# Optimization experiments

Hardware: AMD Instinct MI355X
Metric: run time of the kernel (lower is better)

## Reference

```python
import jax, jax.numpy as jnp
import numpy as np

DIM = 1024
NUM_HEADS = 16
EFF = NUM_HEADS // 2          # 8 effective heads
HEAD_DIM = DIM // NUM_HEADS   # 64
LAMBDA_INIT = 0.8
EPS = 1e-5
B, N = 2, 2048


def setup_inputs() -> dict:
    key = jax.random.key(0)
    ks = jax.random.split(key, 14)
    s = 0.02
    return {
        "x": jax.random.normal(ks[0], (B, N, DIM), jnp.float32),
        "Wq": jax.random.normal(ks[1], (DIM, DIM), jnp.float32) * s,
        "bq": jnp.zeros((DIM,), jnp.float32),
        "Wk": jax.random.normal(ks[2], (DIM, DIM), jnp.float32) * s,
        "bk": jnp.zeros((DIM,), jnp.float32),
        "Wv": jax.random.normal(ks[3], (DIM, DIM), jnp.float32) * s,
        "bv": jnp.zeros((DIM,), jnp.float32),
        "Wo": jax.random.normal(ks[4], (DIM, DIM), jnp.float32) * s,
        "bo": jnp.zeros((DIM,), jnp.float32),
        "g": jnp.ones((2 * HEAD_DIM,), jnp.float32),          # RMSNorm weight
        "lq1": jax.random.normal(ks[5], (HEAD_DIM,), jnp.float32) * 0.1,
        "lk1": jax.random.normal(ks[6], (HEAD_DIM,), jnp.float32) * 0.1,
        "lq2": jax.random.normal(ks[7], (HEAD_DIM,), jnp.float32) * 0.1,
        "lk2": jax.random.normal(ks[8], (HEAD_DIM,), jnp.float32) * 0.1,
    }


def reference(x, Wq, bq, Wk, bk, Wv, bv, Wo, bo, g, lq1, lk1, lq2, lk2):
    b, n, d = x.shape
    scaling = HEAD_DIM ** -0.5

    q = x @ Wq + bq                                  # (B,N,D)
    k = x @ Wk + bk
    v = x @ Wv + bv

    # split into 2*EFF heads of HEAD_DIM for q,k; EFF heads of 2*HEAD_DIM for v
    q = q.reshape(b, n, 2 * EFF, HEAD_DIM).transpose(0, 2, 1, 3) * scaling
    k = k.reshape(b, n, 2 * EFF, HEAD_DIM).transpose(0, 2, 1, 3)
    v = v.reshape(b, n, EFF, 2 * HEAD_DIM).transpose(0, 2, 1, 3)

    scores = jnp.einsum('bhnd,bhmd->bhnm', q, k)     # (B,2*EFF,N,N)
    probs = jax.nn.softmax(scores, axis=-1)
    probs = probs.reshape(b, EFF, 2, n, n)           # pair adjacent heads

    lam1 = jnp.exp(jnp.sum(lq1 * lk1))
    lam2 = jnp.exp(jnp.sum(lq2 * lk2))
    lam = lam1 - lam2 + LAMBDA_INIT

    diff = probs[:, :, 0] - lam * probs[:, :, 1]     # (B,EFF,N,N)
    out = jnp.einsum('bhnm,bhmd->bhnd', diff, v)     # (B,EFF,N,2*HEAD_DIM)

    # headwise RMSNorm over last dim (2*HEAD_DIM), in float32
    rms = jax.lax.rsqrt(jnp.mean(out * out, axis=-1, keepdims=True) + EPS)
    out = out * rms * g
    out = out * (1.0 - LAMBDA_INIT)

    out = out.transpose(0, 2, 1, 3).reshape(b, n, d)
    return out @ Wo + bo
```

## Files before the change

### kernel.cpp

```cpp
#include <hip/hip_runtime.h>


typedef unsigned short bf16;
typedef __attribute__((ext_vector_type(8))) short bf16x8;
typedef __attribute__((ext_vector_type(4))) float f32x4;

#define B_SZ   2
#define SEQ    2048
#define DMODEL 1024
#define NH     16
#define NEFF   8

__device__ __forceinline__ bf16 f2b(float f) {
  union { float f; unsigned int u; } c; c.f = f;
  unsigned int lsb = (c.u >> 16) & 1u;
  c.u += 0x7fffu + lsb;
  return (bf16)(c.u >> 16);
}

__device__ __forceinline__ void gll16(const void* g, void* l) {
  __builtin_amdgcn_global_load_lds(
      (const __attribute__((address_space(1))) void*)g,
      (__attribute__((address_space(3))) void*)l, 16, 0, 0);
}

__device__ __forceinline__ bf16x8 frag_swz(const bf16* tile, int row, int e) {
  const int idx = (row << 6) + (((e >> 3) ^ (row & 7)) << 3) + (e & 7);
  return *(const bf16x8*)(tile + idx);
}


__global__ void cast4_kernel(const float* __restrict__ in, bf16* __restrict__ out, int n4) {
  int i = blockIdx.x * blockDim.x + threadIdx.x;
  if (i >= n4) return;
  float4 v = reinterpret_cast<const float4*>(in)[i];
  unsigned long long r = (unsigned long long)f2b(v.x)
                       | ((unsigned long long)f2b(v.y) << 16)
                       | ((unsigned long long)f2b(v.z) << 32)
                       | ((unsigned long long)f2b(v.w) << 48);
  reinterpret_cast<unsigned long long*>(out)[i] = r;
}

__global__ void transpose_cast4_kernel(const float* __restrict__ W0, const float* __restrict__ W1,
                                       const float* __restrict__ W2, const float* __restrict__ W3,
                                       bf16* __restrict__ dqkv, bf16* __restrict__ dwo) {
  __shared__ float tile[64][65];
  const int z = blockIdx.z;
  const float* in = (z == 0) ? W0 : (z == 1) ? W1 : (z == 2) ? W2 : W3;
  bf16* out = (z < 3) ? (dqkv + (size_t)z * 1024 * 1024) : dwo;
  const int tx = threadIdx.x & 63;
  const int ty = threadIdx.x >> 6;
  const int bx = blockIdx.x << 6;
  const int by = blockIdx.y << 6;
  #pragma unroll
  for (int r = ty; r < 64; r += 4)
    tile[r][tx] = in[(size_t)(by + r) * DMODEL + bx + tx];
  __syncthreads();
  #pragma unroll
  for (int r = ty; r < 64; r += 4)
    out[(size_t)(bx + r) * DMODEL + by + tx] = f2b(tile[tx][r]);
}

__global__ void lambda_kernel(const float* lq1, const float* lk1,
                              const float* lq2, const float* lk2, float* out) {
  int l = threadIdx.x;
  float p1 = lq1[l] * lk1[l];
  float p2 = lq2[l] * lk2[l];
  #pragma unroll
  for (int off = 32; off; off >>= 1) {
    p1 += __shfl_down(p1, off, 64);
    p2 += __shfl_down(p2, off, 64);
  }
  if (l == 0) out[0] = __expf(p1) - __expf(p2) + 0.8f;
}

__launch_bounds__(256, 3)
__global__ void gemm_qkv(const bf16* __restrict__ A, const bf16* __restrict__ BT,
                         const float* __restrict__ bq, const float* __restrict__ bk,
                         const float* __restrict__ bv,
                         bf16* __restrict__ Qb, bf16* __restrict__ Kb, bf16* __restrict__ Vt) {
  __shared__ __align__(16) bf16 Asl[128][64];
  __shared__ __align__(16) bf16 Bsl[128][64];
  const int tid = threadIdx.x;
  const int wid = tid >> 6;
  const int lane = tid & 63;
  const int li = lane & 15;
  const int lg = lane >> 4;
  const int wm = (wid >> 1) << 6;
  const int wn = (wid & 1) << 6;
  const int bm = blockIdx.x << 7;
  const int bn = blockIdx.y << 7;
  const int sr = lane >> 3;
  const int scs = ((lane & 7) ^ sr) << 3;
  const bf16* Ag = A + ((size_t)bm << 10);
  const bf16* Bg = BT + ((size_t)bn << 10);
  f32x4 acc[4][4] = {};

  for (int k0 = 0; k0 < DMODEL; k0 += 64) {
    #pragma unroll
    for (int pass = 0; pass < 4; ++pass) {
      const int rb = (wid << 5) + (pass << 3);
      const int r = rb + sr;
      gll16(Ag + ((size_t)r << 10) + k0 + scs, &Asl[rb][0]);
      gll16(Bg + ((size_t)r << 10) + k0 + scs, &Bsl[rb][0]);
    }
    __syncthreads();
    #pragma unroll
    for (int kk = 0; kk < 2; ++kk) {
      bf16x8 af[4], bfx[4];
      #pragma unroll
      for (int mi = 0; mi < 4; ++mi)
        af[mi] = frag_swz(&Asl[0][0], wm + (mi << 4) + li, (kk << 5) + (lg << 3));
      #pragma unroll
      for (int ni = 0; ni < 4; ++ni)
        bfx[ni] = frag_swz(&Bsl[0][0], wn + (ni << 4) + li, (kk << 5) + (lg << 3));
      #pragma unroll
      for (int mi = 0; mi < 4; ++mi)
        #pragma unroll
        for (int ni = 0; ni < 4; ++ni)
          acc[mi][ni] = __builtin_amdgcn_mfma_f32_16x16x32_bf16(af[mi], bfx[ni], acc[mi][ni], 0, 0, 0);
    }
    __syncthreads();
  }

  const int seg = bn >> 10;
  #pragma unroll
  for (int ni = 0; ni < 4; ++ni) {
    const int gcol = bn + wn + (ni << 4) + li;
    const int c = gcol & 1023;
    const float bb = (seg == 0 ? bq : seg == 1 ? bk : bv)[c];
    #pragma unroll
    for (int mi = 0; mi < 4; ++mi) {
      const int rbase = bm + wm + (mi << 4) + (lg << 2);
      #pragma unroll
      for (int r = 0; r < 4; ++r) {
        const int grow = rbase + r;
        const int b = grow >> 11, n = grow & 2047;
        float v = acc[mi][ni][r] + bb;
        if (seg == 0) {
          v *= 0.18033688f;
          const int h = c >> 6, d = c & 63;
          Qb[((((size_t)(b * NH + h) << 11) + n) << 6) + d] = f2b(v);
        } else if (seg == 1) {
          const int h = c >> 6, d = c & 63;
          Kb[((((size_t)(b * NH + h) << 11) + n) << 6) + d] = f2b(v);
        } else {
          const int j = c >> 7, d = c & 127;
          Vt[((((size_t)(b * NEFF + j) << 7) + d) << 11) + n] = f2b(v);
        }
      }
    }
  }
}

__launch_bounds__(256, 2)
__global__ void gemm_out(const bf16* __restrict__ A, const bf16* __restrict__ BT,
                         const float* __restrict__ bias, float* __restrict__ out) {
  __shared__ __align__(16) bf16 Asl[64][64];
  __shared__ __align__(16) bf16 Bsl[128][64];
  const int tid = threadIdx.x;
  const int wid = tid >> 6;
  const int lane = tid & 63;
  const int li = lane & 15;
  const int lg = lane >> 4;
  const int wm = (wid >> 1) << 5;
  const int wn = (wid & 1) << 6;
  const int bm = blockIdx.x << 6;
  const int bn = blockIdx.y << 7;
  const int sr = lane >> 3;
  const int scs = ((lane & 7) ^ sr) << 3;
  const bf16* Ag = A + ((size_t)bm << 10);
  const bf16* Bg = BT + ((size_t)bn << 10);
  f32x4 acc[2][4] = {};

  for (int k0 = 0; k0 < DMODEL; k0 += 64) {
    #pragma unroll
    for (int pass = 0; pass < 2; ++pass) {
      const int rb = (wid << 4) + (pass << 3);
      const int r = rb + sr;
      gll16(Ag + ((size_t)r << 10) + k0 + scs, &Asl[rb][0]);
    }
    #pragma unroll
    for (int pass = 0; pass < 4; ++pass) {
      const int rb = (wid << 5) + (pass << 3);
      const int r = rb + sr;
      gll16(Bg + ((size_t)r << 10) + k0 + scs, &Bsl[rb][0]);
    }
    __syncthreads();
    #pragma unroll
    for (int kk = 0; kk < 2; ++kk) {
      bf16x8 af[2], bfx[4];
      #pragma unroll
      for (int mi = 0; mi < 2; ++mi)
        af[mi] = frag_swz(&Asl[0][0], wm + (mi << 4) + li, (kk << 5) + (lg << 3));
      #pragma unroll
      for (int ni = 0; ni < 4; ++ni)
        bfx[ni] = frag_swz(&Bsl[0][0], wn + (ni << 4) + li, (kk << 5) + (lg << 3));
      #pragma unroll
      for (int mi = 0; mi < 2; ++mi)
        #pragma unroll
        for (int ni = 0; ni < 4; ++ni)
          acc[mi][ni] = __builtin_amdgcn_mfma_f32_16x16x32_bf16(af[mi], bfx[ni], acc[mi][ni], 0, 0, 0);
    }
    __syncthreads();
  }

  #pragma unroll
  for (int ni = 0; ni < 4; ++ni) {
    const int gcol = bn + wn + (ni << 4) + li;
    const float bb = bias[gcol];
    #pragma unroll
    for (int mi = 0; mi < 2; ++mi) {
      const int rbase = bm + wm + (mi << 4) + (lg << 2);
      #pragma unroll
      for (int r = 0; r < 4; ++r) {
        const int grow = rbase + r;
        out[((size_t)grow << 10) + gcol] = acc[mi][ni][r] + bb;
      }
    }
  }
}

__launch_bounds__(256, 2)
__global__ void diff_attn(const bf16* __restrict__ Qb, const bf16* __restrict__ Kb,
                          const bf16* __restrict__ Vt, const float* __restrict__ gw,
                          const float* __restrict__ lam_p, bf16* __restrict__ attn_out) {
  __shared__ __align__(16) bf16 K0s[2][64][64];
  __shared__ __align__(16) bf16 K1s[2][64][64];
  __shared__ __align__(16) bf16 Vts[2][128][64];
  __shared__ __align__(16) bf16 Ps[4][2][16][64];

  const int tid = threadIdx.x;
  const int wid = tid >> 6;
  const int lane = tid & 63;
  const int li = lane & 15;
  const int lg = lane >> 4;

  const int bid = blockIdx.x;
  const int xcd = bid & 7;
  const int i6 = bid >> 3;
  const int p = (xcd << 1) + (i6 >> 5);
  const int q0 = (i6 & 31) << 6;
  const int b = p >> 3, j = p & 7;
  const int h0 = 2 * j, h1 = 2 * j + 1;

  const int sr = lane >> 3;
  const int scs = (((lane & 7) ^ sr)) << 3;

  const int qrow = q0 + (wid << 4) + li;
  const bf16* Q0g = Qb + ((((size_t)(b * NH + h0) << 11) + qrow) << 6);
  const bf16* Q1g = Qb + ((((size_t)(b * NH + h1) << 11) + qrow) << 6);
  bf16x8 aq0[2], aq1[2];
  aq0[0] = *(const bf16x8*)(Q0g + (lg << 3));
  aq0[1] = *(const bf16x8*)(Q0g + 32 + (lg << 3));
  aq1[0] = *(const bf16x8*)(Q1g + (lg << 3));
  aq1[1] = *(const bf16x8*)(Q1g + 32 + (lg << 3));

  const bf16* K0g = Kb + ((size_t)(b * NH + h0) << 17);
  const bf16* K1g = Kb + ((size_t)(b * NH + h1) << 17);
  const bf16* Vg  = Vt + ((size_t)p << 18);

  f32x4 o0[8] = {}, o1[8] = {};
  f32x4 ol0 = {}, ol1 = {};
  const bf16x8 vones = {0x3F80, 0x3F80, 0x3F80, 0x3F80, 0x3F80, 0x3F80, 0x3F80, 0x3F80};

  auto stage = [&](int bi, int t) {
    const int kv0 = t << 6;
    #pragma unroll
    for (int pass = 0; pass < 2; ++pass) {
      const int rl = (pass << 5) + (wid << 3) + sr;
      gll16(K0g + ((size_t)(kv0 + rl) << 6) + scs, &K0s[bi][(pass << 5) + (wid << 3)][0]);
      gll16(K1g + ((size_t)(kv0 + rl) << 6) + scs, &K1s[bi][(pass << 5) + (wid << 3)][0]);
    }
    #pragma unroll
    for (int pass = 0; pass < 4; ++pass) {
      const int d = (pass << 5) + (wid << 3) + sr;
      gll16(Vg + ((size_t)d << 11) + kv0 + scs, &Vts[bi][(pass << 5) + (wid << 3)][0]);
    }
  };

  const int NT = SEQ / 64;
  stage(0, 0);
  __syncthreads();

  for (int t = 0; t < NT; ++t) {
    const int cur = t & 1;
    if (t + 1 < NT) stage(cur ^ 1, t + 1);

    f32x4 s0[4] = {}, s1[4] = {};
    __builtin_amdgcn_s_setprio(1);
    #pragma unroll
    for (int kk = 0; kk < 2; ++kk) {
      #pragma unroll
      for (int ni = 0; ni < 4; ++ni) {
        bf16x8 bk0 = frag_swz(&K0s[cur][0][0], (ni << 4) + li, (kk << 5) + (lg << 3));
        s0[ni] = __builtin_amdgcn_mfma_f32_16x16x32_bf16(aq0[kk], bk0, s0[ni], 0, 0, 0);
        bf16x8 bk1 = frag_swz(&K1s[cur][0][0], (ni << 4) + li, (kk << 5) + (lg << 3));
        s1[ni] = __builtin_amdgcn_mfma_f32_16x16x32_bf16(aq1[kk], bk1, s1[ni], 0, 0, 0);
      }
    }
    __builtin_amdgcn_s_setprio(0);

    #pragma unroll
    for (int ni = 0; ni < 4; ++ni) {
      #pragma unroll
      for (int r = 0; r < 4; ++r) {
        const int pr = (lg << 2) + r;
        const int cs = ((ni << 4) + li) ^ ((pr & 7) << 3);
        Ps[wid][0][pr][cs] = f2b(__builtin_amdgcn_exp2f(s0[ni][r] - 12.0f));
        Ps[wid][1][pr][cs] = f2b(__builtin_amdgcn_exp2f(s1[ni][r] - 12.0f));
      }
    }
    bf16x8 pa0[2], pa1[2];
    pa0[0] = frag_swz(&Ps[wid][0][0][0], li, (lg << 3));
    pa0[1] = frag_swz(&Ps[wid][0][0][0], li, 32 + (lg << 3));
    pa1[0] = frag_swz(&Ps[wid][1][0][0], li, (lg << 3));
    pa1[1] = frag_swz(&Ps[wid][1][0][0], li, 32 + (lg << 3));
    __builtin_amdgcn_s_setprio(1);
    #pragma unroll
    for (int kk = 0; kk < 2; ++kk) {
      #pragma unroll
      for (int vc = 0; vc < 8; ++vc) {
        bf16x8 bv = frag_swz(&Vts[cur][0][0], (vc << 4) + li, (kk << 5) + (lg << 3));
        o0[vc] = __builtin_amdgcn_mfma_f32_16x16x32_bf16(pa0[kk], bv, o0[vc], 0, 0, 0);
        o1[vc] = __builtin_amdgcn_mfma_f32_16x16x32_bf16(pa1[kk], bv, o1[vc], 0, 0, 0);
      }
      ol0 = __builtin_amdgcn_mfma_f32_16x16x32_bf16(pa0[kk], vones, ol0, 0, 0, 0);
      ol1 = __builtin_amdgcn_mfma_f32_16x16x32_bf16(pa1[kk], vones, ol1, 0, 0, 0);
    }
    __builtin_amdgcn_s_setprio(0);
    __syncthreads();
  }

  const float lam = lam_p[0];
  float inv0[4], inv1[4];
  #pragma unroll
  for (int r = 0; r < 4; ++r) { inv0[r] = 1.f / ol0[r]; inv1[r] = 1.f / ol1[r]; }
  float ov[8][4];
  float ss[4] = {0.f, 0.f, 0.f, 0.f};
  #pragma unroll
  for (int vc = 0; vc < 8; ++vc)
    #pragma unroll
    for (int r = 0; r < 4; ++r) {
      const float v = o0[vc][r] * inv0[r] - lam * o1[vc][r] * inv1[r];
      ov[vc][r] = v;
      ss[r] += v * v;
    }
  #pragma unroll
  for (int r = 0; r < 4; ++r) {
    float v = ss[r];
    #pragma unroll
    for (int off = 1; off < 16; off <<= 1) v += __shfl_xor(v, off, 64);
    ss[r] = rsqrtf(v * (1.f / 128.f) + 1e-5f);
  }
  #pragma unroll
  for (int vc = 0; vc < 8; ++vc) {
    const float gv = gw[(vc << 4) + li];
    #pragma unroll
    for (int r = 0; r < 4; ++r) {
      const int row = q0 + (wid << 4) + (lg << 2) + r;
      const float v = ov[vc][r] * ss[r] * gv * 0.2f;
      attn_out[(((size_t)(b << 11) + row) << 10) + (j << 7) + (vc << 4) + li] = f2b(v);
    }
  }
}


extern "C" void kernel_launch(void* const* d_in, const int* in_sizes, int n_in,
                              void* d_out, int out_size, void* d_ws, size_t ws_size,
                              hipStream_t stream) {
  (void)in_sizes; (void)n_in; (void)out_size; (void)ws_size;
  const float* x   = (const float*)d_in[0];
  const float* Wq  = (const float*)d_in[1];
  const float* bq  = (const float*)d_in[2];
  const float* Wk  = (const float*)d_in[3];
  const float* bk  = (const float*)d_in[4];
  const float* Wv  = (const float*)d_in[5];
  const float* bv  = (const float*)d_in[6];
  const float* Wo  = (const float*)d_in[7];
  const float* bo  = (const float*)d_in[8];
  const float* g   = (const float*)d_in[9];
  const float* lq1 = (const float*)d_in[10];
  const float* lk1 = (const float*)d_in[11];
  const float* lq2 = (const float*)d_in[12];
  const float* lk2 = (const float*)d_in[13];

  char* ws = (char*)d_ws;
  const size_t MB = 1024 * 1024;
  bf16* xb    = (bf16*)(ws + 0 * MB);
  bf16* WqkvT = (bf16*)(ws + 8 * MB);
  bf16* WoT   = (bf16*)(ws + 14 * MB);
  bf16* Qb    = (bf16*)(ws + 16 * MB);
  bf16* Kb    = (bf16*)(ws + 24 * MB);
  bf16* Vt    = (bf16*)(ws + 32 * MB);
  bf16* attn  = (bf16*)(ws + 40 * MB);
  float* lam  = (float*)(ws + 48 * MB);

  cast4_kernel<<<4096, 256, 0, stream>>>(x, xb, (B_SZ * SEQ * DMODEL) / 4);
  transpose_cast4_kernel<<<dim3(16, 16, 4), 256, 0, stream>>>(Wq, Wk, Wv, Wo, WqkvT, WoT);
  lambda_kernel<<<1, 64, 0, stream>>>(lq1, lk1, lq2, lk2, lam);

  gemm_qkv<<<dim3(32, 24), 256, 0, stream>>>(xb, WqkvT, bq, bk, bv, Qb, Kb, Vt);
  diff_attn<<<512, 256, 0, stream>>>(Qb, Kb, Vt, g, lam, attn);
  gemm_out<<<dim3(64, 8), 256, 0, stream>>>(attn, WoT, bo, (float*)d_out);
}
```

Before: 147.4 us.

## Split each KV tile across two wave groups in diff attention, reduce via LDS

The attention kernel now launches 512 threads per block instead of 256. The two halves of each 64-key tile are handled by separate groups of four waves, each computing scores and PV products for 32 keys. After the loop, the partial O accumulators and row sums from the second group are added into the first group's registers through LDS, in several synchronized phases. This doubles the waves per block to raise occupancy and latency hiding, but adds a cross-wave reduction and extra barriers at the end.

```diff
diff --git a/kernel.cpp b/kernel.cpp
--- a/kernel.cpp
+++ b/kernel.cpp
@@ -221,20 +221,25 @@
   }
 }
 
-__launch_bounds__(256, 2)
+__launch_bounds__(512, 4)
 __global__ void diff_attn(const bf16* __restrict__ Qb, const bf16* __restrict__ Kb,
                           const bf16* __restrict__ Vt, const float* __restrict__ gw,
                           const float* __restrict__ lam_p, bf16* __restrict__ attn_out) {
   __shared__ __align__(16) bf16 K0s[2][64][64];
   __shared__ __align__(16) bf16 K1s[2][64][64];
   __shared__ __align__(16) bf16 Vts[2][128][64];
-  __shared__ __align__(16) bf16 Ps[4][2][16][64];
+  __shared__ __align__(16) char PsRaw[16384];
+
+  bf16* Pb = (bf16*)PsRaw;
+  float* xf = (float*)PsRaw;
 
   const int tid = threadIdx.x;
   const int wid = tid >> 6;
   const int lane = tid & 63;
   const int li = lane & 15;
   const int lg = lane >> 4;
+  const int slice = wid & 3;
+  const int kvh = wid >> 2;
 
   const int bid = blockIdx.x;
   const int xcd = bid & 7;
@@ -247,7 +252,7 @@
   const int sr = lane >> 3;
   const int scs = (((lane & 7) ^ sr)) << 3;
 
-  const int qrow = q0 + (wid << 4) + li;
+  const int qrow = q0 + (slice << 4) + li;
   const bf16* Q0g = Qb + ((((size_t)(b * NH + h0) << 11) + qrow) << 6);
   const bf16* Q1g = Qb + ((((size_t)(b * NH + h1) << 11) + qrow) << 6);
   bf16x8 aq0[2], aq1[2];
@@ -266,19 +271,17 @@
 
   auto stage = [&](int bi, int t) {
     const int kv0 = t << 6;
+    const int rl = (wid << 3) + sr;
+    gll16(K0g + ((size_t)(kv0 + rl) << 6) + scs, &K0s[bi][wid << 3][0]);
+    gll16(K1g + ((size_t)(kv0 + rl) << 6) + scs, &K1s[bi][wid << 3][0]);
     #pragma unroll
     for (int pass = 0; pass < 2; ++pass) {
-      const int rl = (pass << 5) + (wid << 3) + sr;
-      gll16(K0g + ((size_t)(kv0 + rl) << 6) + scs, &K0s[bi][(pass << 5) + (wid << 3)][0]);
-      gll16(K1g + ((size_t)(kv0 + rl) << 6) + scs, &K1s[bi][(pass << 5) + (wid << 3)][0]);
-    }
-    #pragma unroll
-    for (int pass = 0; pass < 4; ++pass) {
-      const int d = (pass << 5) + (wid << 3) + sr;
-      gll16(Vg + ((size_t)d << 11) + kv0 + scs, &Vts[bi][(pass << 5) + (wid << 3)][0]);
+      const int d = (pass << 6) + (wid << 3) + sr;
+      gll16(Vg + ((size_t)d << 11) + kv0 + scs, &Vts[bi][(pass << 6) + (wid << 3)][0]);
     }
   };
 
+  const int pbase = wid << 10;
   const int NT = SEQ / 64;
   stage(0, 0);
   __syncthreads();
@@ -287,80 +290,133 @@
     const int cur = t & 1;
     if (t + 1 < NT) stage(cur ^ 1, t + 1);
 
-    f32x4 s0[4] = {}, s1[4] = {};
+    f32x4 s0[2] = {}, s1[2] = {};
     __builtin_amdgcn_s_setprio(1);
     #pragma unroll
     for (int kk = 0; kk < 2; ++kk) {
       #pragma unroll
-      for (int ni = 0; ni < 4; ++ni) {
-        bf16x8 bk0 = frag_swz(&K0s[cur][0][0], (ni << 4) + li, (kk << 5) + (lg << 3));
+      for (int ni = 0; ni < 2; ++ni) {
+        const int rowB = (kvh << 5) + (ni << 4) + li;
+        bf16x8 bk0 = frag_swz(&K0s[cur][0][0], rowB, (kk << 5) + (lg << 3));
         s0[ni] = __builtin_amdgcn_mfma_f32_16x16x32_bf16(aq0[kk], bk0, s0[ni], 0, 0, 0);
-        bf16x8 bk1 = frag_swz(&K1s[cur][0][0], (ni << 4) + li, (kk << 5) + (lg << 3));
+        bf16x8 bk1 = frag_swz(&K1s[cur][0][0], rowB, (kk << 5) + (lg << 3));
         s1[ni] = __builtin_amdgcn_mfma_f32_16x16x32_bf16(aq1[kk], bk1, s1[ni], 0, 0, 0);
       }
     }
     __builtin_amdgcn_s_setprio(0);
 
     #pragma unroll
-    for (int ni = 0; ni < 4; ++ni) {
+    for (int ni = 0; ni < 2; ++ni) {
       #pragma unroll
       for (int r = 0; r < 4; ++r) {
         const int pr = (lg << 2) + r;
-        const int cs = ((ni << 4) + li) ^ ((pr & 7) << 3);
-        Ps[wid][0][pr][cs] = f2b(__builtin_amdgcn_exp2f(s0[ni][r] - 12.0f));
-        Ps[wid][1][pr][cs] = f2b(__builtin_amdgcn_exp2f(s1[ni][r] - 12.0f));
-      }
-    }
-    bf16x8 pa0[2], pa1[2];
-    pa0[0] = frag_swz(&Ps[wid][0][0][0], li, (lg << 3));
-    pa0[1] = frag_swz(&Ps[wid][0][0][0], li, 32 + (lg << 3));
-    pa1[0] = frag_swz(&Ps[wid][1][0][0], li, (lg << 3));
-    pa1[1] = frag_swz(&Ps[wid][1][0][0], li, 32 + (lg << 3));
+        const int col = (ni << 4) + li;
+        const int idx = (pr << 5) + ((((col >> 3) ^ (pr >> 2)) & 3) << 3) + (col & 7);
+        Pb[pbase + idx]       = f2b(__builtin_amdgcn_exp2f(s0[ni][r] - 12.0f));
+        Pb[pbase + 512 + idx] = f2b(__builtin_amdgcn_exp2f(s1[ni][r] - 12.0f));
+      }
+    }
+    const int ridx = (li << 5) + (((lg ^ (li >> 2)) & 3) << 3);
+    bf16x8 pa0 = *(const bf16x8*)(Pb + pbase + ridx);
+    bf16x8 pa1 = *(const bf16x8*)(Pb + pbase + 512 + ridx);
+
     __builtin_amdgcn_s_setprio(1);
     #pragma unroll
-    for (int kk = 0; kk < 2; ++kk) {
-      #pragma unroll
-      for (int vc = 0; vc < 8; ++vc) {
-        bf16x8 bv = frag_swz(&Vts[cur][0][0], (vc << 4) + li, (kk << 5) + (lg << 3));
-        o0[vc] = __builtin_amdgcn_mfma_f32_16x16x32_bf16(pa0[kk], bv, o0[vc], 0, 0, 0);
-        o1[vc] = __builtin_amdgcn_mfma_f32_16x16x32_bf16(pa1[kk], bv, o1[vc], 0, 0, 0);
-      }
-      ol0 = __builtin_amdgcn_mfma_f32_16x16x32_bf16(pa0[kk], vones, ol0, 0, 0, 0);
-      ol1 = __builtin_amdgcn_mfma_f32_16x16x32_bf16(pa1[kk], vones, ol1, 0, 0, 0);
-    }
+    for (int vc = 0; vc < 8; ++vc) {
+      bf16x8 bv = frag_swz(&Vts[cur][0][0], (vc << 4) + li, (kvh << 5) + (lg << 3));
+      o0[vc] = __builtin_amdgcn_mfma_f32_16x16x32_bf16(pa0, bv, o0[vc], 0, 0, 0);
+      o1[vc] = __builtin_amdgcn_mfma_f32_16x16x32_bf16(pa1, bv, o1[vc], 0, 0, 0);
+    }
+    ol0 = __builtin_amdgcn_mfma_f32_16x16x32_bf16(pa0, vones, ol0, 0, 0, 0);
+    ol1 = __builtin_amdgcn_mfma_f32_16x16x32_bf16(pa1, vones, ol1, 0, 0, 0);
     __builtin_amdgcn_s_setprio(0);
     __syncthreads();
   }
 
-  const float lam = lam_p[0];
-  float inv0[4], inv1[4];
-  #pragma unroll
-  for (int r = 0; r < 4; ++r) { inv0[r] = 1.f / ol0[r]; inv1[r] = 1.f / ol1[r]; }
-  float ov[8][4];
-  float ss[4] = {0.f, 0.f, 0.f, 0.f};
-  #pragma unroll
-  for (int vc = 0; vc < 8; ++vc)
+  #pragma unroll
+  for (int half = 0; half < 2; ++half) {
+    __syncthreads();
+    if (kvh == 1 && (slice >> 1) == half) {
+      #pragma unroll
+      for (int vc = 0; vc < 8; ++vc)
+        #pragma unroll
+        for (int r = 0; r < 4; ++r)
+          xf[((((slice & 1) << 4) + (lg << 2) + r) << 7) + (vc << 4) + li] = o0[vc][r];
+    }
+    __syncthreads();
+    if (kvh == 0 && (slice >> 1) == half) {
+      #pragma unroll
+      for (int vc = 0; vc < 8; ++vc)
+        #pragma unroll
+        for (int r = 0; r < 4; ++r)
+          o0[vc][r] += xf[((((slice & 1) << 4) + (lg << 2) + r) << 7) + (vc << 4) + li];
+    }
+  }
+  #pragma unroll
+  for (int half = 0; half < 2; ++half) {
+    __syncthreads();
+    if (kvh == 1 && (slice >> 1) == half) {
+      #pragma unroll
+      for (int vc = 0; vc < 8; ++vc)
+        #pragma unroll
+        for (int r = 0; r < 4; ++r)
+          xf[((((slice & 1) << 4) + (lg << 2) + r) << 7) + (vc << 4) + li] = o1[vc][r];
+    }
+    __syncthreads();
+    if (kvh == 0 && (slice >> 1) == half) {
+      #pragma unroll
+      for (int vc = 0; vc < 8; ++vc)
+        #pragma unroll
+        for (int r = 0; r < 4; ++r)
+          o1[vc][r] += xf[((((slice & 1) << 4) + (lg << 2) + r) << 7) + (vc << 4) + li];
+    }
+  }
+  __syncthreads();
+  if (kvh == 1 && li == 0) {
     #pragma unroll
     for (int r = 0; r < 4; ++r) {
-      const float v = o0[vc][r] * inv0[r] - lam * o1[vc][r] * inv1[r];
-      ov[vc][r] = v;
-      ss[r] += v * v;
-    }
-  #pragma unroll
-  for (int r = 0; r < 4; ++r) {
-    float v = ss[r];
-    #pragma unroll
-    for (int off = 1; off < 16; off <<= 1) v += __shfl_xor(v, off, 64);
-    ss[r] = rsqrtf(v * (1.f / 128.f) + 1e-5f);
-  }
-  #pragma unroll
-  for (int vc = 0; vc < 8; ++vc) {
-    const float gv = gw[(vc << 4) + li];
+      xf[(slice << 5) + (lg << 2) + r]      = ol0[r];
+      xf[(slice << 5) + 16 + (lg << 2) + r] = ol1[r];
+    }
+  }
+  __syncthreads();
+
+  if (kvh == 0) {
     #pragma unroll
     for (int r = 0; r < 4; ++r) {
-      const int row = q0 + (wid << 4) + (lg << 2) + r;
-      const float v = ov[vc][r] * ss[r] * gv * 0.2f;
-      attn_out[(((size_t)(b << 11) + row) << 10) + (j << 7) + (vc << 4) + li] = f2b(v);
+      ol0[r] += xf[(slice << 5) + (lg << 2) + r];
+      ol1[r] += xf[(slice << 5) + 16 + (lg << 2) + r];
+    }
+    const float lam = lam_p[0];
+    float inv0[4], inv1[4];
+    #pragma unroll
+    for (int r = 0; r < 4; ++r) { inv0[r] = 1.f / ol0[r]; inv1[r] = 1.f / ol1[r]; }
+    float ov[8][4];
+    float ss[4] = {0.f, 0.f, 0.f, 0.f};
+    #pragma unroll
+    for (int vc = 0; vc < 8; ++vc)
+      #pragma unroll
+      for (int r = 0; r < 4; ++r) {
+        const float v = o0[vc][r] * inv0[r] - lam * o1[vc][r] * inv1[r];
+        ov[vc][r] = v;
+        ss[r] += v * v;
+      }
+    #pragma unroll
+    for (int r = 0; r < 4; ++r) {
+      float v = ss[r];
+      #pragma unroll
+      for (int off = 1; off < 16; off <<= 1) v += __shfl_xor(v, off, 64);
+      ss[r] = rsqrtf(v * (1.f / 128.f) + 1e-5f);
+    }
+    #pragma unroll
+    for (int vc = 0; vc < 8; ++vc) {
+      const float gv = gw[(vc << 4) + li];
+      #pragma unroll
+      for (int r = 0; r < 4; ++r) {
+        const int row = q0 + (slice << 4) + (lg << 2) + r;
+        const float v = ov[vc][r] * ss[r] * gv * 0.2f;
+        attn_out[(((size_t)(b << 11) + row) << 10) + (j << 7) + (vc << 4) + li] = f2b(v);
+      }
     }
   }
 }
@@ -401,6 +457,6 @@
   lambda_kernel<<<1, 64, 0, stream>>>(lq1, lk1, lq2, lk2, lam);
 
   gemm_qkv<<<dim3(32, 24), 256, 0, stream>>>(xb, WqkvT, bq, bk, bv, Qb, Kb, Vt);
-  diff_attn<<<512, 256, 0, stream>>>(Qb, Kb, Vt, g, lam, attn);
+  diff_attn<<<512, 512, 0, stream>>>(Qb, Kb, Vt, g, lam, attn);
   gemm_out<<<dim3(64, 8), 256, 0, stream>>>(attn, WoT, bo, (float*)d_out);
 }
```

Result: slower. 171.4 us (+16.3%).

## Merge prep kernels into one launch and shrink output GEMM M-tile

Applied to the files above, without the earlier changes.

Three small preprocessing kernels (x cast, weight transpose-cast, lambda reduction) are merged into a single launch that dispatches on block index, removing two kernel launches and the gaps between them. Separately, the output projection GEMM tile is halved in M (64 to 32 rows), doubling the grid to 1024 blocks and raising the occupancy hint to 4, so the 256-CU device gets more blocks to spread. The smaller tile lowers data reuse per block, since each WoT tile is loaded twice as often.

```diff
diff --git a/kernel.cpp b/kernel.cpp
--- a/kernel.cpp
+++ b/kernel.cpp
@@ -29,49 +29,53 @@
   return *(const bf16x8*)(tile + idx);
 }
 
-
-__global__ void cast4_kernel(const float* __restrict__ in, bf16* __restrict__ out, int n4) {
-  int i = blockIdx.x * blockDim.x + threadIdx.x;
-  if (i >= n4) return;
-  float4 v = reinterpret_cast<const float4*>(in)[i];
-  unsigned long long r = (unsigned long long)f2b(v.x)
-                       | ((unsigned long long)f2b(v.y) << 16)
-                       | ((unsigned long long)f2b(v.z) << 32)
-                       | ((unsigned long long)f2b(v.w) << 48);
-  reinterpret_cast<unsigned long long*>(out)[i] = r;
-}
-
-__global__ void transpose_cast4_kernel(const float* __restrict__ W0, const float* __restrict__ W1,
-                                       const float* __restrict__ W2, const float* __restrict__ W3,
-                                       bf16* __restrict__ dqkv, bf16* __restrict__ dwo) {
-  __shared__ float tile[64][65];
-  const int z = blockIdx.z;
-  const float* in = (z == 0) ? W0 : (z == 1) ? W1 : (z == 2) ? W2 : W3;
-  bf16* out = (z < 3) ? (dqkv + (size_t)z * 1024 * 1024) : dwo;
-  const int tx = threadIdx.x & 63;
-  const int ty = threadIdx.x >> 6;
-  const int bx = blockIdx.x << 6;
-  const int by = blockIdx.y << 6;
-  #pragma unroll
-  for (int r = ty; r < 64; r += 4)
-    tile[r][tx] = in[(size_t)(by + r) * DMODEL + bx + tx];
-  __syncthreads();
-  #pragma unroll
-  for (int r = ty; r < 64; r += 4)
-    out[(size_t)(bx + r) * DMODEL + by + tx] = f2b(tile[tx][r]);
-}
-
-__global__ void lambda_kernel(const float* lq1, const float* lk1,
-                              const float* lq2, const float* lk2, float* out) {
-  int l = threadIdx.x;
-  float p1 = lq1[l] * lk1[l];
-  float p2 = lq2[l] * lk2[l];
-  #pragma unroll
-  for (int off = 32; off; off >>= 1) {
-    p1 += __shfl_down(p1, off, 64);
-    p2 += __shfl_down(p2, off, 64);
-  }
-  if (l == 0) out[0] = __expf(p1) - __expf(p2) + 0.8f;
+__global__ void prep_kernel(const float* __restrict__ x, bf16* __restrict__ xb,
+                            const float* __restrict__ W0, const float* __restrict__ W1,
+                            const float* __restrict__ W2, const float* __restrict__ W3,
+                            bf16* __restrict__ dqkv, bf16* __restrict__ dwo,
+                            const float* __restrict__ lq1, const float* __restrict__ lk1,
+                            const float* __restrict__ lq2, const float* __restrict__ lk2,
+                            float* __restrict__ lam) {
+  const int bid = blockIdx.x;
+  const int tid = threadIdx.x;
+  if (bid < 4096) {
+    const int i = (bid << 8) + tid;
+    float4 v = reinterpret_cast<const float4*>(x)[i];
+    unsigned long long r = (unsigned long long)f2b(v.x)
+                         | ((unsigned long long)f2b(v.y) << 16)
+                         | ((unsigned long long)f2b(v.z) << 32)
+                         | ((unsigned long long)f2b(v.w) << 48);
+    reinterpret_cast<unsigned long long*>(xb)[i] = r;
+  } else if (bid < 5120) {
+    __shared__ float tile[64][65];
+    const int t = bid - 4096;
+    const int z = t >> 8;
+    const int tz = t & 255;
+    const float* in = (z == 0) ? W0 : (z == 1) ? W1 : (z == 2) ? W2 : W3;
+    bf16* out = (z < 3) ? (dqkv + (size_t)z * 1024 * 1024) : dwo;
+    const int tx = tid & 63;
+    const int ty = tid >> 6;
+    const int bx = (tz & 15) << 6;
+    const int by = (tz >> 4) << 6;
+    #pragma unroll
+    for (int r = ty; r < 64; r += 4)
+      tile[r][tx] = in[(size_t)(by + r) * DMODEL + bx + tx];
+    __syncthreads();
+    #pragma unroll
+    for (int r = ty; r < 64; r += 4)
+      out[(size_t)(bx + r) * DMODEL + by + tx] = f2b(tile[tx][r]);
+  } else {
+    if (tid < 64) {
+      float p1 = lq1[tid] * lk1[tid];
+      float p2 = lq2[tid] * lk2[tid];
+      #pragma unroll
+      for (int off = 32; off; off >>= 1) {
+        p1 += __shfl_down(p1, off, 64);
+        p2 += __shfl_down(p2, off, 64);
+      }
+      if (tid == 0) lam[0] = __expf(p1) - __expf(p2) + 0.8f;
+    }
+  }
 }
 
 __launch_bounds__(256, 3)
@@ -153,30 +157,29 @@
   }
 }
 
-__launch_bounds__(256, 2)
+__launch_bounds__(256, 4)
 __global__ void gemm_out(const bf16* __restrict__ A, const bf16* __restrict__ BT,
                          const float* __restrict__ bias, float* __restrict__ out) {
-  __shared__ __align__(16) bf16 Asl[64][64];
+  __shared__ __align__(16) bf16 Asl[32][64];
   __shared__ __align__(16) bf16 Bsl[128][64];
   const int tid = threadIdx.x;
   const int wid = tid >> 6;
   const int lane = tid & 63;
   const int li = lane & 15;
   const int lg = lane >> 4;
-  const int wm = (wid >> 1) << 5;
+  const int wm = (wid >> 1) << 4;
   const int wn = (wid & 1) << 6;
-  const int bm = blockIdx.x << 6;
+  const int bm = blockIdx.x << 5;
   const int bn = blockIdx.y << 7;
   const int sr = lane >> 3;
   const int scs = ((lane & 7) ^ sr) << 3;
   const bf16* Ag = A + ((size_t)bm << 10);
   const bf16* Bg = BT + ((size_t)bn << 10);
-  f32x4 acc[2][4] = {};
+  f32x4 acc[4] = {};
 
   for (int k0 = 0; k0 < DMODEL; k0 += 64) {
-    #pragma unroll
-    for (int pass = 0; pass < 2; ++pass) {
-      const int rb = (wid << 4) + (pass << 3);
+    {
+      const int rb = wid << 3;
       const int r = rb + sr;
       gll16(Ag + ((size_t)r << 10) + k0 + scs, &Asl[rb][0]);
     }
@@ -189,18 +192,14 @@
     __syncthreads();
     #pragma unroll
     for (int kk = 0; kk < 2; ++kk) {
-      bf16x8 af[2], bfx[4];
-      #pragma unroll
-      for (int mi = 0; mi < 2; ++mi)
-        af[mi] = frag_swz(&Asl[0][0], wm + (mi << 4) + li, (kk << 5) + (lg << 3));
+      bf16x8 af = frag_swz(&Asl[0][0], wm + li, (kk << 5) + (lg << 3));
+      bf16x8 bfx[4];
       #pragma unroll
       for (int ni = 0; ni < 4; ++ni)
         bfx[ni] = frag_swz(&Bsl[0][0], wn + (ni << 4) + li, (kk << 5) + (lg << 3));
       #pragma unroll
-      for (int mi = 0; mi < 2; ++mi)
-        #pragma unroll
-        for (int ni = 0; ni < 4; ++ni)
-          acc[mi][ni] = __builtin_amdgcn_mfma_f32_16x16x32_bf16(af[mi], bfx[ni], acc[mi][ni], 0, 0, 0);
+      for (int ni = 0; ni < 4; ++ni)
+        acc[ni] = __builtin_amdgcn_mfma_f32_16x16x32_bf16(af, bfx[ni], acc[ni], 0, 0, 0);
     }
     __syncthreads();
   }
@@ -209,14 +208,11 @@
   for (int ni = 0; ni < 4; ++ni) {
     const int gcol = bn + wn + (ni << 4) + li;
     const float bb = bias[gcol];
-    #pragma unroll
-    for (int mi = 0; mi < 2; ++mi) {
-      const int rbase = bm + wm + (mi << 4) + (lg << 2);
-      #pragma unroll
-      for (int r = 0; r < 4; ++r) {
-        const int grow = rbase + r;
-        out[((size_t)grow << 10) + gcol] = acc[mi][ni][r] + bb;
-      }
+    const int rbase = bm + wm + (lg << 2);
+    #pragma unroll
+    for (int r = 0; r < 4; ++r) {
+      const int grow = rbase + r;
+      out[((size_t)grow << 10) + gcol] = acc[ni][r] + bb;
     }
   }
 }
@@ -396,11 +392,9 @@
   bf16* attn  = (bf16*)(ws + 40 * MB);
   float* lam  = (float*)(ws + 48 * MB);
 
-  cast4_kernel<<<4096, 256, 0, stream>>>(x, xb, (B_SZ * SEQ * DMODEL) / 4);
-  transpose_cast4_kernel<<<dim3(16, 16, 4), 256, 0, stream>>>(Wq, Wk, Wv, Wo, WqkvT, WoT);
-  lambda_kernel<<<1, 64, 0, stream>>>(lq1, lk1, lq2, lk2, lam);
-
+  prep_kernel<<<5121, 256, 0, stream>>>(x, xb, Wq, Wk, Wv, Wo, WqkvT, WoT,
+                                        lq1, lk1, lq2, lk2, lam);
   gemm_qkv<<<dim3(32, 24), 256, 0, stream>>>(xb, WqkvT, bq, bk, bv, Qb, Kb, Vt);
   diff_attn<<<512, 256, 0, stream>>>(Qb, Kb, Vt, g, lam, attn);
-  gemm_out<<<dim3(64, 8), 256, 0, stream>>>(attn, WoT, bo, (float*)d_out);
-}
+  gemm_out<<<dim3(128, 8), 256, 0, stream>>>(attn, WoT, bo, (float*)d_out);
+}
```

Measured after the change: 142.6 us. 1.03x faster.
